# Kernel optimization log

Measured on AMD Instinct MI355X. Metric: run time of the kernel, lower is better.

The kernel has to match this reference:

```python
import jax, jax.numpy as jnp
import numpy as np

B, S, D = 16, 2048, 64
K, M = 8, 2048

def setup_inputs() -> dict:
    key = jax.random.key(0)
    kx, kc = jax.random.split(key)
    x = jax.random.normal(kx, (B, S, D), dtype=jnp.float32)
    # nn.init.uniform_(weight, -1/M, 1/M)
    codebooks = jax.random.uniform(kc, (K, M, D), dtype=jnp.float32,
                                   minval=-1.0 / M, maxval=1.0 / M)
    return {"x": x, "codebooks": codebooks}

def reference(x, codebooks):
    """Residual VQ: sequentially quantize residual against K codebooks.

    x: (B,S,D) float32; codebooks: (K,M,D) float32.
    Returns (quantized (B,S,D), indices (K,B,S) int32).
    Uses squared-distance expansion ||r||^2 - 2 r.c + ||c||^2 (argmin-equivalent
    to torch.norm) to avoid materializing the (B,S,M,D) difference tensor.
    """
    def step(residual, cb):  # residual: (B,S,D), cb: (M,D)
        r2 = jnp.sum(residual * residual, axis=-1, keepdims=True)   # (B,S,1)
        c2 = jnp.sum(cb * cb, axis=-1)                              # (M,)
        cross = jnp.einsum('bsd,md->bsm', residual, cb)             # (B,S,M)
        d2 = r2 - 2.0 * cross + c2                                  # (B,S,M)
        idx = jnp.argmin(d2, axis=-1)                               # (B,S)
        q = cb[idx]                                                 # (B,S,D) gather
        return residual - q, idx

    residual, indices = jax.lax.scan(step, x, codebooks)
    quantized = x - residual
    return quantized, indices
```

## Files before the change

kernel.cpp:

```cpp
#include <hip/hip_runtime.h>


#define BB 16
#define SS 2048
#define DD 64
#define KK 8
#define MM 2048
#define NPTS (BB * SS)
#define QSIZE (NPTS * DD)
#define NCHUNK 8
#define WPB 8
#define PPB 512
#define MCHUNK (MM / NCHUNK)

__global__ __launch_bounds__(256) void rvq_prep(const float* __restrict__ cb,
                                                float* __restrict__ c2,
                                                unsigned long long* __restrict__ keys) {
#pragma clang fp contract(off)
    int tid = blockIdx.x * 256 + threadIdx.x;
    const float* row = cb + (size_t)tid * DD;
    float r[8];
#pragma unroll
    for (int j = 0; j < 8; ++j) { float v = row[j]; r[j] = v * v; }
#pragma unroll
    for (int i = 8; i < DD; i += 8) {
#pragma unroll
        for (int j = 0; j < 8; ++j) { float v = row[i + j]; float t = v * v; r[j] += t; }
    }
    c2[tid] = ((r[0] + r[1]) + (r[2] + r[3])) + ((r[4] + r[5]) + (r[6] + r[7]));
    keys[tid] = ~0ULL;
    keys[tid + KK * MM] = ~0ULL;
}

#define R2K(A, B, C, E) \
    "v_pk_mul_f32 v[92:93], v[" A "], v[" A "]\n\t" \
    "v_pk_add_f32 v[80:81], v[80:81], v[92:93]\n\t" \
    "v_pk_mul_f32 v[92:93], v[" B "], v[" B "]\n\t" \
    "v_pk_add_f32 v[82:83], v[82:83], v[92:93]\n\t" \
    "v_pk_mul_f32 v[92:93], v[" C "], v[" C "]\n\t" \
    "v_pk_add_f32 v[84:85], v[84:85], v[92:93]\n\t" \
    "v_pk_mul_f32 v[92:93], v[" E "], v[" E "]\n\t" \
    "v_pk_add_f32 v[86:87], v[86:87], v[92:93]\n\t"

#define GRP(SA, SB, VA, VB) \
    "v_pk_mul_f32 v[84:85], s[" SA "], v[" VA "]\n\t" \
    "v_pk_mul_f32 v[86:87], s[" SB "], v[" VB "]\n\t" \
    "v_pk_add_f32 v[80:81], v[80:81], v[84:85]\n\t" \
    "v_pk_add_f32 v[82:83], v[82:83], v[86:87]\n\t"

#define GRPL(CA, CB, VA, VB) \
    "v_pk_mul_f32 v[84:85], v[" CA "], v[" VA "]\n\t" \
    "v_pk_mul_f32 v[86:87], v[" CB "], v[" VB "]\n\t" \
    "v_pk_add_f32 v[80:81], v[80:81], v[84:85]\n\t" \
    "v_pk_add_f32 v[82:83], v[82:83], v[86:87]\n\t"

#define SMEMLD(BA, BB, C2D) \
    "s_min_u32 s30, s29, 0xff00\n\t" \
    "s_load_dwordx16 s[" BA "], %[cb], s30\n\t" \
    "s_add_u32 s25, s30, 64\n\t" \
    "s_load_dwordx16 s[" BB "], %[cb], s25\n\t" \
    "s_lshr_b32 s25, s30, 6\n\t" \
    "s_load_dword " C2D ", %[c2], s25\n\t" \
    "s_add_u32 s29, s29, 256\n\t"

#define DSLD \
    "ds_read_b128 v[96:99],   v94\n\t" \
    "ds_read_b128 v[100:103], v94 offset:16\n\t" \
    "ds_read_b128 v[104:107], v94 offset:32\n\t" \
    "ds_read_b128 v[108:111], v94 offset:48\n\t" \
    "ds_read_b128 v[112:115], v94 offset:64\n\t" \
    "ds_read_b128 v[116:119], v94 offset:80\n\t" \
    "ds_read_b128 v[120:123], v94 offset:96\n\t" \
    "ds_read_b128 v[124:127], v94 offset:112\n\t" \
    "v_add_u32 v94, 0x80, v94\n\t" \
    "v_min_u32 v94, v95, v94\n\t"

#define EINL \
    GRPL("108:109","110:111","60:61","62:63") \
    GRPL("104:105","106:107","56:57","58:59") \
    GRPL("100:101","102:103","52:53","54:55") \
    GRPL("96:97","98:99","48:49","50:51") \
    GRPL("124:125","126:127","76:77","78:79") \
    GRPL("120:121","122:123","72:73","74:75") \
    GRPL("116:117","118:119","68:69","70:71") \
    GRPL("112:113","114:115","64:65","66:67")

#define EINP \
    "v_pk_mul_f32 v[80:81], s[44:45], v[28:29]\n\t" \
    "v_pk_mul_f32 v[82:83], s[46:47], v[30:31]\n\t" \
    GRP("40:41","42:43","24:25","26:27") \
    GRP("36:37","38:39","20:21","22:23") \
    GRP("32:33","34:35","16:17","18:19") \
    GRP("60:61","62:63","44:45","46:47") \
    GRP("56:57","58:59","40:41","42:43") \
    GRP("52:53","54:55","36:37","38:39") \
    GRP("48:49","50:51","32:33","34:35") \
    EINL

#define EINQ \
    "v_pk_mul_f32 v[80:81], s[76:77], v[28:29]\n\t" \
    "v_pk_mul_f32 v[82:83], s[78:79], v[30:31]\n\t" \
    GRP("72:73","74:75","24:25","26:27") \
    GRP("68:69","70:71","20:21","22:23") \
    GRP("64:65","66:67","16:17","18:19") \
    GRP("92:93","94:95","44:45","46:47") \
    GRP("88:89","90:91","40:41","42:43") \
    GRP("84:85","86:87","36:37","38:39") \
    GRP("80:81","82:83","32:33","34:35") \
    EINL

#define FINX(C2S) \
    "v_add_f32 v92, v80, v81\n\t" \
    "v_add_f32 v93, v82, v83\n\t" \
    "v_add_f32 v92, v92, v93\n\t" \
    "v_fma_f32 v92, v92, -2.0, v88\n\t" \
    "v_add_f32 v92, " C2S ", v92\n\t" \
    "v_cmp_lt_f32 vcc, v92, v89\n\t" \
    "v_cndmask_b32 v89, v89, v92, vcc\n\t" \
    "v_cndmask_b32 v90, v90, v91, vcc\n\t" \
    "v_add_u32 v91, 1, v91\n\t"

__global__ __launch_bounds__(512, 4) void rvq_main(const float* __restrict__ res_in,
                                                   const float* __restrict__ cbk,
                                                   const float* __restrict__ c2k,
                                                   unsigned long long* __restrict__ keys) {
#pragma clang fp contract(off)
    const int tid = threadIdx.x;
    const int lane = tid & 63;
    const int wv = __builtin_amdgcn_readfirstlane(tid >> 6);
    const int ch = blockIdx.x & (NCHUNK - 1);
    const int bp = blockIdx.x >> 3;
    const int point = bp * PPB + wv * 64 + lane;

    const int m0 = ch * MCHUNK;
    const float* cbw = cbk + (size_t)m0 * DD;
    const float* c2w = c2k + m0;
    const unsigned long long ra = (unsigned long long)(res_in + (size_t)point * DD);

    __shared__ __align__(16) float lds_cb[MCHUNK * 32];
    for (int i = tid; i < MCHUNK * 8; i += PPB) {
        const int row = i >> 3;
        const int o = (i & 7) << 2;
        *(float4*)&lds_cb[row * 32 + o] = *(const float4*)(cbw + row * DD + 32 + o);
    }
    __syncthreads();
    const unsigned ldsbase = (unsigned)(unsigned long long)(void*)&lds_cb[0];
    const unsigned ldsclamp = ldsbase + (MCHUNK - 1) * 128;

    float best;
    int bidx;
    asm volatile(
        "global_load_dwordx4 v[16:19], %[ra], off\n\t"
        "global_load_dwordx4 v[20:23], %[ra], off offset:16\n\t"
        "global_load_dwordx4 v[24:27], %[ra], off offset:32\n\t"
        "global_load_dwordx4 v[28:31], %[ra], off offset:48\n\t"
        "global_load_dwordx4 v[32:35], %[ra], off offset:64\n\t"
        "global_load_dwordx4 v[36:39], %[ra], off offset:80\n\t"
        "global_load_dwordx4 v[40:43], %[ra], off offset:96\n\t"
        "global_load_dwordx4 v[44:47], %[ra], off offset:112\n\t"
        "global_load_dwordx4 v[48:51], %[ra], off offset:128\n\t"
        "global_load_dwordx4 v[52:55], %[ra], off offset:144\n\t"
        "global_load_dwordx4 v[56:59], %[ra], off offset:160\n\t"
        "global_load_dwordx4 v[60:63], %[ra], off offset:176\n\t"
        "global_load_dwordx4 v[64:67], %[ra], off offset:192\n\t"
        "global_load_dwordx4 v[68:71], %[ra], off offset:208\n\t"
        "global_load_dwordx4 v[72:75], %[ra], off offset:224\n\t"
        "global_load_dwordx4 v[76:79], %[ra], off offset:240\n\t"
        "s_waitcnt vmcnt(0)\n\t"
        "v_pk_mul_f32 v[80:81], v[16:17], v[16:17]\n\t"
        "v_pk_mul_f32 v[82:83], v[18:19], v[18:19]\n\t"
        "v_pk_mul_f32 v[84:85], v[20:21], v[20:21]\n\t"
        "v_pk_mul_f32 v[86:87], v[22:23], v[22:23]\n\t"
        R2K("24:25", "26:27", "28:29", "30:31")
        R2K("32:33", "34:35", "36:37", "38:39")
        R2K("40:41", "42:43", "44:45", "46:47")
        R2K("48:49", "50:51", "52:53", "54:55")
        R2K("56:57", "58:59", "60:61", "62:63")
        R2K("64:65", "66:67", "68:69", "70:71")
        R2K("72:73", "74:75", "76:77", "78:79")
        "v_add_f32 v92, v80, v81\n\t"
        "v_add_f32 v93, v82, v83\n\t"
        "v_add_f32 v92, v92, v93\n\t"
        "v_add_f32 v93, v84, v85\n\t"
        "v_add_f32 v88, v86, v87\n\t"
        "v_add_f32 v93, v93, v88\n\t"
        "v_add_f32 v88, v92, v93\n\t"
        "v_mov_b32 v89, 0x7f800000\n\t"
        "v_mov_b32 v90, 0\n\t"
        "v_mov_b32 v91, %[m0]\n\t"
        "v_mov_b32 v94, %[lb]\n\t"
        "v_mov_b32 v95, %[lc]\n\t"
        "s_mov_b32 s29, 0\n\t"
        SMEMLD("32:47", "48:63", "s26")
        DSLD
        "s_mov_b32 s24, 0\n\t"
        "Ltop_%=:\n\t"
        "s_waitcnt lgkmcnt(0)\n\t"
        SMEMLD("64:79", "80:95", "s27")
        EINP
        DSLD
        FINX("s26")
        "s_waitcnt lgkmcnt(0)\n\t"
        SMEMLD("32:47", "48:63", "s26")
        EINQ
        DSLD
        FINX("s27")
        "s_add_u32 s24, s24, 1\n\t"
        "s_cmp_lg_u32 s24, 128\n\t"
        "s_cbranch_scc1 Ltop_%=\n\t"
        "s_waitcnt lgkmcnt(0)\n\t"
        "v_mov_b32 %[ob], v89\n\t"
        "v_mov_b32 %[oi], v90\n\t"
        : [ob] "=v"(best), [oi] "=v"(bidx)
        : [ra] "v"(ra), [cb] "s"(cbw), [c2] "s"(c2w), [m0] "s"(m0),
          [lb] "s"(ldsbase), [lc] "s"(ldsclamp)
        : "vcc", "scc",
          "s24","s25","s26","s27","s29","s30",
          "s32","s33","s34","s35","s36","s37","s38","s39",
          "s40","s41","s42","s43","s44","s45","s46","s47","s48","s49","s50","s51",
          "s52","s53","s54","s55","s56","s57","s58","s59","s60","s61","s62","s63",
          "s64","s65","s66","s67","s68","s69","s70","s71","s72","s73","s74","s75",
          "s76","s77","s78","s79","s80","s81","s82","s83","s84","s85","s86","s87",
          "s88","s89","s90","s91","s92","s93","s94","s95",
          "v16","v17","v18","v19","v20","v21","v22","v23","v24","v25","v26","v27",
          "v28","v29","v30","v31","v32","v33","v34","v35","v36","v37","v38","v39",
          "v40","v41","v42","v43","v44","v45","v46","v47","v48","v49","v50","v51",
          "v52","v53","v54","v55","v56","v57","v58","v59","v60","v61","v62","v63",
          "v64","v65","v66","v67","v68","v69","v70","v71","v72","v73","v74","v75",
          "v76","v77","v78","v79","v80","v81","v82","v83","v84","v85","v86","v87",
          "v88","v89","v90","v91","v92","v93","v94","v95","v96","v97","v98","v99",
          "v100","v101","v102","v103","v104","v105","v106","v107","v108","v109",
          "v110","v111","v112","v113","v114","v115","v116","v117","v118","v119",
          "v120","v121","v122","v123","v124","v125","v126","v127");

    unsigned long long key =
        ((unsigned long long)__float_as_uint(best) << 32) | (unsigned int)bidx;
    atomicMin(&keys[point], key);
}

__global__ __launch_bounds__(256) void rvq_update(const float* __restrict__ res_in,
                                                  float* __restrict__ res_out,
                                                  const float* __restrict__ x,
                                                  const float* __restrict__ cbk,
                                                  unsigned long long* __restrict__ keys,
                                                  float* __restrict__ idx_out,
                                                  int last) {
#pragma clang fp contract(off)
    __shared__ unsigned long long sk[4];
    const int tid = threadIdx.x;
    const int e = blockIdx.x * 256 + tid;
    const int p0 = blockIdx.x * 4;
    if (tid < 4) {
        unsigned long long k = keys[p0 + tid];
        sk[tid] = k;
        keys[p0 + tid] = ~0ULL;
        idx_out[p0 + tid] = (float)(unsigned int)k;
    }
    __syncthreads();
    const int pi = tid >> 6;
    const int d = tid & 63;
    const int m = (int)(unsigned int)sk[pi];
    const float r = res_in[e] - cbk[(size_t)m * DD + d];
    if (last) res_out[e] = x[e] - r;
    else      res_out[e] = r;
}

extern "C" void kernel_launch(void* const* d_in, const int* in_sizes, int n_in,
                              void* d_out, int out_size, void* d_ws, size_t ws_size,
                              hipStream_t stream) {
    const float* x  = (const float*)d_in[0];
    const float* cb = (const float*)d_in[1];

    float* out = (float*)d_out;
    float* quant = out;
    float* idx_out = out + QSIZE;

    float* c2   = (float*)d_ws;
    float* res1 = c2 + (size_t)KK * MM;
    unsigned long long* keys =
        (unsigned long long*)(res1 + (size_t)QSIZE);
    float* R[2] = { quant, res1 };

    rvq_prep<<<(KK * MM) / 256, 256, 0, stream>>>(cb, c2, keys);

    for (int k = 0; k < KK; ++k) {
        const float* rin = (k == 0) ? x : R[(k - 1) & 1];
        const int last = (k == KK - 1);
        float* rout = last ? quant : R[k & 1];
        rvq_main<<<(NPTS / PPB) * NCHUNK, PPB, 0, stream>>>(
            rin,
            cb + (size_t)k * MM * DD,
            c2 + (size_t)k * MM,
            keys);
        rvq_update<<<QSIZE / 256, 256, 0, stream>>>(
            rin, rout, x,
            cb + (size_t)k * MM * DD,
            keys,
            idx_out + (size_t)k * NPTS,
            last);
    }
}
```

Measured before the change: 1.317 ms.

## Rebalance codebook operand split between scalar loads and LDS with packed chunks

The prep kernel now copies each codebook chunk into a packed buffer with its squared norms appended, so one scalar base pointer covers both codes and norms. The main loop changes the split of each code pair: more dimensions are fed from scalar registers (48 of 64 for one code, 32 for the other) and only the remainder comes from a compact 48-float-per-pair LDS layout. Scalar loads and LDS reads are interleaved with the math to overlap latency. This cuts LDS traffic and footprint per code, in exchange for more scalar-memory bandwidth, an extra copy of the codebooks, and more intricate hand-scheduled assembly.

```diff
diff --git a/kernel.cpp b/kernel.cpp
--- a/kernel.cpp
+++ b/kernel.cpp
@@ -12,13 +12,19 @@
 #define WPB 8
 #define PPB 512
 #define MCHUNK (MM / NCHUNK)
+#define PACKF 16640
 
 __global__ __launch_bounds__(256) void rvq_prep(const float* __restrict__ cb,
-                                                float* __restrict__ c2,
+                                                float* __restrict__ pack,
                                                 unsigned long long* __restrict__ keys) {
 #pragma clang fp contract(off)
-    int tid = blockIdx.x * 256 + threadIdx.x;
-    const float* row = cb + (size_t)tid * DD;
+    const int b = blockIdx.x;
+    const int tid = threadIdx.x;
+    const float* src = cb + (size_t)b * 16384;
+    float* dst = pack + (size_t)b * PACKF;
+    for (int i = tid; i < 4096; i += 256)
+        *(float4*)&dst[i * 4] = *(const float4*)&src[i * 4];
+    const float* row = src + (size_t)tid * DD;
     float r[8];
 #pragma unroll
     for (int j = 0; j < 8; ++j) { float v = row[j]; r[j] = v * v; }
@@ -27,9 +33,9 @@
 #pragma unroll
         for (int j = 0; j < 8; ++j) { float v = row[i + j]; float t = v * v; r[j] += t; }
     }
-    c2[tid] = ((r[0] + r[1]) + (r[2] + r[3])) + ((r[4] + r[5]) + (r[6] + r[7]));
-    keys[tid] = ~0ULL;
-    keys[tid + KK * MM] = ~0ULL;
+    dst[16384 + tid] = ((r[0] + r[1]) + (r[2] + r[3])) + ((r[4] + r[5]) + (r[6] + r[7]));
+    keys[b * 512 + tid] = ~0ULL;
+    keys[b * 512 + 256 + tid] = ~0ULL;
 }
 
 #define R2K(A, B, C, E) \
@@ -54,38 +60,27 @@
     "v_pk_add_f32 v[80:81], v[80:81], v[84:85]\n\t" \
     "v_pk_add_f32 v[82:83], v[82:83], v[86:87]\n\t"
 
-#define SMEMLD(BA, BB, C2D) \
-    "s_min_u32 s30, s29, 0xff00\n\t" \
-    "s_load_dwordx16 s[" BA "], %[cb], s30\n\t" \
-    "s_add_u32 s25, s30, 64\n\t" \
-    "s_load_dwordx16 s[" BB "], %[cb], s25\n\t" \
-    "s_lshr_b32 s25, s30, 6\n\t" \
-    "s_load_dword " C2D ", %[c2], s25\n\t" \
-    "s_add_u32 s29, s29, 256\n\t"
-
-#define DSLD \
-    "ds_read_b128 v[96:99],   v94\n\t" \
-    "ds_read_b128 v[100:103], v94 offset:16\n\t" \
-    "ds_read_b128 v[104:107], v94 offset:32\n\t" \
-    "ds_read_b128 v[108:111], v94 offset:48\n\t" \
-    "ds_read_b128 v[112:115], v94 offset:64\n\t" \
-    "ds_read_b128 v[116:119], v94 offset:80\n\t" \
-    "ds_read_b128 v[120:123], v94 offset:96\n\t" \
-    "ds_read_b128 v[124:127], v94 offset:112\n\t" \
-    "v_add_u32 v94, 0x80, v94\n\t" \
-    "v_min_u32 v94, v95, v94\n\t"
-
-#define EINL \
-    GRPL("108:109","110:111","60:61","62:63") \
-    GRPL("104:105","106:107","56:57","58:59") \
-    GRPL("100:101","102:103","52:53","54:55") \
-    GRPL("96:97","98:99","48:49","50:51") \
-    GRPL("124:125","126:127","76:77","78:79") \
-    GRPL("120:121","122:123","72:73","74:75") \
-    GRPL("116:117","118:119","68:69","70:71") \
-    GRPL("112:113","114:115","64:65","66:67")
-
-#define EINP \
+#define SMEM_B_ISSUE \
+    "s_add_u32 s15, s14, 0x100\n\t" \
+    "s_load_dwordx16 s[16:31], %[pb], s15\n\t" \
+    "s_add_u32 s15, s15, 0x40\n\t" \
+    "s_load_dwordx16 s[80:95], %[pb], s15\n\t"
+
+#define SMEM_A_NEXT \
+    "s_add_u32 s15, s14, 0x200\n\t" \
+    "s_min_u32 s15, s15, 0xfe00\n\t" \
+    "s_load_dwordx16 s[32:47], %[pb], s15\n\t" \
+    "s_add_u32 s15, s15, 0x40\n\t" \
+    "s_load_dwordx16 s[48:63], %[pb], s15\n\t" \
+    "s_add_u32 s15, s15, 0x40\n\t" \
+    "s_load_dwordx16 s[64:79], %[pb], s15\n\t"
+
+#define C2_NEXT \
+    "s_lshr_b32 s15, s15, 6\n\t" \
+    "s_add_u32 s15, s15, 0xfffe\n\t" \
+    "s_load_dwordx2 s[12:13], %[pb], s15\n\t"
+
+#define EINSM_A \
     "v_pk_mul_f32 v[80:81], s[44:45], v[28:29]\n\t" \
     "v_pk_mul_f32 v[82:83], s[46:47], v[30:31]\n\t" \
     GRP("40:41","42:43","24:25","26:27") \
@@ -95,19 +90,54 @@
     GRP("56:57","58:59","40:41","42:43") \
     GRP("52:53","54:55","36:37","38:39") \
     GRP("48:49","50:51","32:33","34:35") \
-    EINL
-
-#define EINQ \
-    "v_pk_mul_f32 v[80:81], s[76:77], v[28:29]\n\t" \
-    "v_pk_mul_f32 v[82:83], s[78:79], v[30:31]\n\t" \
-    GRP("72:73","74:75","24:25","26:27") \
-    GRP("68:69","70:71","20:21","22:23") \
-    GRP("64:65","66:67","16:17","18:19") \
+    GRP("76:77","78:79","60:61","62:63") \
+    GRP("72:73","74:75","56:57","58:59") \
+    GRP("68:69","70:71","52:53","54:55") \
+    GRP("64:65","66:67","48:49","50:51")
+
+#define TAIL_A \
+    GRPL("108:109","110:111","76:77","78:79") \
+    GRPL("104:105","106:107","72:73","74:75") \
+    GRPL("100:101","102:103","68:69","70:71") \
+    GRPL("96:97","98:99","64:65","66:67")
+
+#define DS_B \
+    "ds_read_b128 v[96:99],   v94 offset:64\n\t" \
+    "ds_read_b128 v[100:103], v94 offset:80\n\t" \
+    "ds_read_b128 v[104:107], v94 offset:96\n\t" \
+    "ds_read_b128 v[108:111], v94 offset:112\n\t" \
+    "ds_read_b128 v[112:115], v94 offset:128\n\t" \
+    "ds_read_b128 v[116:119], v94 offset:144\n\t" \
+    "ds_read_b128 v[120:123], v94 offset:160\n\t" \
+    "ds_read_b128 v[124:127], v94 offset:176\n\t"
+
+#define EINSM_B \
+    "v_pk_mul_f32 v[80:81], s[28:29], v[28:29]\n\t" \
+    "v_pk_mul_f32 v[82:83], s[30:31], v[30:31]\n\t" \
+    GRP("24:25","26:27","24:25","26:27") \
+    GRP("20:21","22:23","20:21","22:23") \
+    GRP("16:17","18:19","16:17","18:19") \
     GRP("92:93","94:95","44:45","46:47") \
     GRP("88:89","90:91","40:41","42:43") \
     GRP("84:85","86:87","36:37","38:39") \
-    GRP("80:81","82:83","32:33","34:35") \
-    EINL
+    GRP("80:81","82:83","32:33","34:35")
+
+#define B_B32_THEN_DSA \
+    GRPL("108:109","110:111","60:61","62:63") \
+    GRPL("104:105","106:107","56:57","58:59") \
+    GRPL("100:101","102:103","52:53","54:55") \
+    GRPL("96:97","98:99","48:49","50:51") \
+    "ds_read_b128 v[96:99],   v94 offset:192\n\t" \
+    "ds_read_b128 v[100:103], v94 offset:208\n\t" \
+    "ds_read_b128 v[104:107], v94 offset:224\n\t" \
+    "ds_read_b128 v[108:111], v94 offset:240\n\t"
+
+#define B_B48 \
+    GRPL("124:125","126:127","76:77","78:79") \
+    GRPL("120:121","122:123","72:73","74:75") \
+    GRPL("116:117","118:119","68:69","70:71") \
+    GRPL("112:113","114:115","64:65","66:67") \
+    "v_add_u32 v94, 0xc0, v94\n\t"
 
 #define FINX(C2S) \
     "v_add_f32 v92, v80, v81\n\t" \
@@ -121,8 +151,7 @@
     "v_add_u32 v91, 1, v91\n\t"
 
 __global__ __launch_bounds__(512, 4) void rvq_main(const float* __restrict__ res_in,
-                                                   const float* __restrict__ cbk,
-                                                   const float* __restrict__ c2k,
+                                                   const float* __restrict__ packk,
                                                    unsigned long long* __restrict__ keys) {
 #pragma clang fp contract(off)
     const int tid = threadIdx.x;
@@ -133,19 +162,19 @@
     const int point = bp * PPB + wv * 64 + lane;
 
     const int m0 = ch * MCHUNK;
-    const float* cbw = cbk + (size_t)m0 * DD;
-    const float* c2w = c2k + m0;
+    const float* pbw = packk + (size_t)ch * PACKF;
     const unsigned long long ra = (unsigned long long)(res_in + (size_t)point * DD);
 
-    __shared__ __align__(16) float lds_cb[MCHUNK * 32];
-    for (int i = tid; i < MCHUNK * 8; i += PPB) {
-        const int row = i >> 3;
-        const int o = (i & 7) << 2;
-        *(float4*)&lds_cb[row * 32 + o] = *(const float4*)(cbw + row * DD + 32 + o);
+    __shared__ __align__(16) float lds_cb[128 * 48 + 48];
+    for (int i = tid; i < 128 * 12; i += PPB) {
+        const int q = i / 12;
+        const int j = i - q * 12;
+        const int row = 2 * q + (j >= 4);
+        const int d = (j < 4) ? (48 + 4 * j) : (16 + 4 * j);
+        *(float4*)&lds_cb[q * 48 + j * 4] = *(const float4*)(pbw + row * DD + d);
     }
     __syncthreads();
     const unsigned ldsbase = (unsigned)(unsigned long long)(void*)&lds_cb[0];
-    const unsigned ldsclamp = ldsbase + (MCHUNK - 1) * 128;
 
     float best;
     int bidx;
@@ -189,34 +218,41 @@
         "v_mov_b32 v90, 0\n\t"
         "v_mov_b32 v91, %[m0]\n\t"
         "v_mov_b32 v94, %[lb]\n\t"
-        "v_mov_b32 v95, %[lc]\n\t"
-        "s_mov_b32 s29, 0\n\t"
-        SMEMLD("32:47", "48:63", "s26")
-        DSLD
-        "s_mov_b32 s24, 0\n\t"
+        "s_mov_b32 s14, 0\n\t"
+        "s_load_dwordx16 s[32:47], %[pb], 0x0\n\t"
+        "s_load_dwordx16 s[48:63], %[pb], 0x40\n\t"
+        "s_load_dwordx16 s[64:79], %[pb], 0x80\n\t"
+        "s_load_dwordx2 s[12:13], %[pb], 0x10000\n\t"
+        "ds_read_b128 v[96:99],   v94\n\t"
+        "ds_read_b128 v[100:103], v94 offset:16\n\t"
+        "ds_read_b128 v[104:107], v94 offset:32\n\t"
+        "ds_read_b128 v[108:111], v94 offset:48\n\t"
         "Ltop_%=:\n\t"
         "s_waitcnt lgkmcnt(0)\n\t"
-        SMEMLD("64:79", "80:95", "s27")
-        EINP
-        DSLD
-        FINX("s26")
+        SMEM_B_ISSUE
+        EINSM_A
+        TAIL_A
+        DS_B
+        FINX("s12")
         "s_waitcnt lgkmcnt(0)\n\t"
-        SMEMLD("32:47", "48:63", "s26")
-        EINQ
-        DSLD
-        FINX("s27")
-        "s_add_u32 s24, s24, 1\n\t"
-        "s_cmp_lg_u32 s24, 128\n\t"
+        SMEM_A_NEXT
+        EINSM_B
+        B_B32_THEN_DSA
+        B_B48
+        FINX("s13")
+        C2_NEXT
+        "s_add_u32 s14, s14, 0x200\n\t"
+        "s_cmp_lg_u32 s14, 0x10000\n\t"
         "s_cbranch_scc1 Ltop_%=\n\t"
         "s_waitcnt lgkmcnt(0)\n\t"
         "v_mov_b32 %[ob], v89\n\t"
         "v_mov_b32 %[oi], v90\n\t"
         : [ob] "=v"(best), [oi] "=v"(bidx)
-        : [ra] "v"(ra), [cb] "s"(cbw), [c2] "s"(c2w), [m0] "s"(m0),
-          [lb] "s"(ldsbase), [lc] "s"(ldsclamp)
+        : [ra] "v"(ra), [pb] "s"(pbw), [m0] "v"(m0), [lb] "v"(ldsbase)
         : "vcc", "scc",
-          "s24","s25","s26","s27","s29","s30",
-          "s32","s33","s34","s35","s36","s37","s38","s39",
+          "s12","s13","s14","s15",
+          "s16","s17","s18","s19","s20","s21","s22","s23","s24","s25","s26","s27",
+          "s28","s29","s30","s31","s32","s33","s34","s35","s36","s37","s38","s39",
           "s40","s41","s42","s43","s44","s45","s46","s47","s48","s49","s50","s51",
           "s52","s53","s54","s55","s56","s57","s58","s59","s60","s61","s62","s63",
           "s64","s65","s66","s67","s68","s69","s70","s71","s72","s73","s74","s75",
@@ -228,7 +264,7 @@
           "v52","v53","v54","v55","v56","v57","v58","v59","v60","v61","v62","v63",
           "v64","v65","v66","v67","v68","v69","v70","v71","v72","v73","v74","v75",
           "v76","v77","v78","v79","v80","v81","v82","v83","v84","v85","v86","v87",
-          "v88","v89","v90","v91","v92","v93","v94","v95","v96","v97","v98","v99",
+          "v88","v89","v90","v91","v92","v93","v94","v96","v97","v98","v99",
           "v100","v101","v102","v103","v104","v105","v106","v107","v108","v109",
           "v110","v111","v112","v113","v114","v115","v116","v117","v118","v119",
           "v120","v121","v122","v123","v124","v125","v126","v127");
@@ -275,13 +311,13 @@
     float* quant = out;
     float* idx_out = out + QSIZE;
 
-    float* c2   = (float*)d_ws;
-    float* res1 = c2 + (size_t)KK * MM;
+    float* res1 = (float*)d_ws;
     unsigned long long* keys =
         (unsigned long long*)(res1 + (size_t)QSIZE);
+    float* pack = (float*)(keys + NPTS);
     float* R[2] = { quant, res1 };
 
-    rvq_prep<<<(KK * MM) / 256, 256, 0, stream>>>(cb, c2, keys);
+    rvq_prep<<<KK * NCHUNK, 256, 0, stream>>>(cb, pack, keys);
 
     for (int k = 0; k < KK; ++k) {
         const float* rin = (k == 0) ? x : R[(k - 1) & 1];
@@ -289,8 +325,7 @@
         float* rout = last ? quant : R[k & 1];
         rvq_main<<<(NPTS / PPB) * NCHUNK, PPB, 0, stream>>>(
             rin,
-            cb + (size_t)k * MM * DD,
-            c2 + (size_t)k * MM,
+            pack + (size_t)k * NCHUNK * PACKF,
             keys);
         rvq_update<<<QSIZE / 256, 256, 0, stream>>>(
             rin, rout, x,
```

Result: no change. 1.309 ms (-0.6%).
